# Kernel tuning notes

Hardware: AMD Instinct MI355X
Metric: run time of the kernel (lower is better)

Reference implementation:

```python
import jax, jax.numpy as jnp
import numpy as np

DT = 0.1
THRESH = 10.0

def setup_inputs() -> dict:
    key = jax.random.key(0)
    ks = jax.random.split(key, 6)
    B, S, H, V = 2, 1024, 1024, 50257
    hidden_states = jax.random.normal(ks[0], (B, S, H), dtype=jnp.float32)
    ttu_state = jnp.zeros((B, 3), dtype=jnp.float32)
    W_imp = jax.random.normal(ks[1], (3, H), dtype=jnp.float32) * 0.02
    b_imp = jnp.zeros((3,), dtype=jnp.float32)
    W_lm = jax.random.normal(ks[2], (V, H), dtype=jnp.float32) * 0.02
    W_mod = jax.random.normal(ks[3], (V, 3), dtype=jnp.float32) * 0.02
    # gamma, alpha_c, beta_c, delta, alpha_d, epsilon, alpha_m
    ttu_params = jax.random.uniform(ks[4], (7,), dtype=jnp.float32, minval=0.1, maxval=1.0)
    return {"hidden_states": hidden_states, "ttu_state": ttu_state,
            "W_imp": W_imp, "b_imp": b_imp, "W_lm": W_lm, "W_mod": W_mod,
            "ttu_params": ttu_params}

def _ttu_scan(ttu_state, impulses, ttu_params):
    # impulses: [S, B, 3] (time-major for scan)
    gamma, alpha_c, beta_c, delta, alpha_d, epsilon, alpha_m = ttu_params
    def step(state, imp):
        phi_c, phi_d, phi_m = state[:, 0], state[:, 1], state[:, 2]
        dphi_c = gamma * imp[:, 0] - alpha_c * phi_c - beta_c * phi_c * phi_d
        dphi_d = delta * phi_c ** 2 - alpha_d * phi_d
        dphi_m = epsilon * phi_d - alpha_m * phi_m
        new_c = phi_c + DT * dphi_c
        new_d = phi_d + DT * dphi_d
        new_m = phi_m + DT * dphi_m
        # saturation damping on phi_d
        new_d = jnp.where(jnp.abs(new_d) > THRESH, jnp.float32(0.5), jnp.float32(1.0)) * new_d
        new_state = jnp.stack([new_c, new_d, new_m], axis=1)  # [B, 3]
        return new_state, new_state
    return jax.lax.scan(step, ttu_state, impulses)

def reference(hidden_states, ttu_state, W_imp, b_imp, W_lm, W_mod, ttu_params):
    # impulse projections computed in batch up front: [S, B, 3]
    impulses = jnp.einsum('bsh,dh->sbd', hidden_states, W_imp) + b_imp
    final_state, states = _ttu_scan(ttu_state, impulses, ttu_params)  # states: [S, B, 3]
    # base lm logits + 0.1 * modulation from ttu trajectory
    logits = jnp.einsum('bsh,vh->bsv', hidden_states, W_lm) \
           + 0.1 * jnp.einsum('sbd,vd->bsv', states, W_mod)
    return logits, final_state
```

## Files before the change

kernel.cpp:

```cpp
#include <hip/hip_runtime.h>
#include <hip/hip_bf16.h>

typedef float  f32x4  __attribute__((ext_vector_type(4)));
typedef float  f32x16 __attribute__((ext_vector_type(16)));
typedef short  bf16x8 __attribute__((ext_vector_type(8)));
typedef short  bf16x4 __attribute__((ext_vector_type(4)));

typedef const void __attribute__((address_space(1))) gv_t;
typedef void __attribute__((address_space(3))) sv_t;

namespace {

constexpr int B_ = 2;
constexpr int S_ = 1024;
constexpr int H_ = 1024;
constexpr int V_ = 50257;
constexpr int M_ = B_ * S_;
constexpr int VP2_ = 50432;
constexpr float DT_ = 0.1f;
constexpr float THRESH_ = 10.0f;

constexpr int BK = 64;
constexpr int NT = H_ / BK;

__device__ __forceinline__ unsigned short f2bf(float f) {
  union { float f; unsigned u; } x;
  x.f = f;
  x.u += 0x7FFFu + ((x.u >> 16) & 1u);
  return (unsigned short)(x.u >> 16);
}

__global__ void cvt_hidden_impulse_kernel(const float* __restrict__ hidden,
                                          const float* __restrict__ W_imp,
                                          const float* __restrict__ b_imp,
                                          unsigned short* __restrict__ hid_bf,
                                          float* __restrict__ imp) {
  const int m = blockIdx.x;
  const int t = threadIdx.x;
  const float4 hv = reinterpret_cast<const float4*>(hidden + (size_t)m * H_)[t];
  const float4 wv = reinterpret_cast<const float4*>(W_imp)[t];
  bf16x4 o;
  o[0] = (short)f2bf(hv.x); o[1] = (short)f2bf(hv.y);
  o[2] = (short)f2bf(hv.z); o[3] = (short)f2bf(hv.w);
  *(bf16x4*)(hid_bf + (size_t)m * H_ + t * 4) = o;
  float p = hv.x * wv.x + hv.y * wv.y + hv.z * wv.z + hv.w * wv.w;
  #pragma unroll
  for (int off = 32; off; off >>= 1) p += __shfl_down(p, off);
  __shared__ float partial[4];
  if ((t & 63) == 0) partial[t >> 6] = p;
  __syncthreads();
  if (t == 0) {
    const float v = partial[0] + partial[1] + partial[2] + partial[3] + b_imp[0];
    const int b = m >> 10;
    const int s = m & (S_ - 1);
    imp[s * B_ + b] = v;
  }
}

__device__ __forceinline__ void scan_body(const float* __restrict__ imp_s,
                                          const float* __restrict__ ttu_state,
                                          const float* __restrict__ ttu_params,
                                          float* __restrict__ states,
                                          float* __restrict__ final_out, int t) {
  if (t < B_) {
    const float gamma   = ttu_params[0];
    const float alpha_c = ttu_params[1];
    const float beta_c  = ttu_params[2];
    const float delta   = ttu_params[3];
    const float alpha_d = ttu_params[4];
    const float epsilon = ttu_params[5];
    const float alpha_m = ttu_params[6];
    float c = ttu_state[t * 3 + 0];
    float d = ttu_state[t * 3 + 1];
    float m = ttu_state[t * 3 + 2];
    for (int s = 0; s < S_; ++s) {
      const float ii = imp_s[s * B_ + t];
      const float dc = gamma * ii - alpha_c * c - beta_c * c * d;
      const float dd = delta * c * c - alpha_d * d;
      const float dm = epsilon * d - alpha_m * m;
      c = c + DT_ * dc;
      float nd = d + DT_ * dd;
      m = m + DT_ * dm;
      nd = (fabsf(nd) > THRESH_ ? 0.5f : 1.0f) * nd;
      d = nd;
      float* st = states + (size_t)(s * B_ + t) * 3;
      st[0] = c; st[1] = d; st[2] = m;
    }
    final_out[t * 3 + 0] = c;
    final_out[t * 3 + 1] = d;
    final_out[t * 3 + 2] = m;
  }
}

__global__ void ttu_scan_kernel(const float* __restrict__ imp,
                                const float* __restrict__ ttu_state,
                                const float* __restrict__ ttu_params,
                                float* __restrict__ states,
                                float* __restrict__ final_out) {
  __shared__ float imp_s[S_ * B_];
  const int t = threadIdx.x;
  for (int i = t; i < S_ * B_; i += 64) imp_s[i] = imp[i];
  __syncthreads();
  scan_body(imp_s, ttu_state, ttu_params, states, final_out, t);
}

__global__ void cvt_wlm_scan_kernel(const float* __restrict__ src,
                                    unsigned short* __restrict__ dst,
                                    long n_src, long n_dst,
                                    const float* __restrict__ imp,
                                    const float* __restrict__ ttu_state,
                                    const float* __restrict__ ttu_params,
                                    float* __restrict__ states,
                                    float* __restrict__ final_out) {
  __shared__ float imp_s[S_ * B_];
  const int t = threadIdx.x;
  if (blockIdx.x == gridDim.x - 1) {
    for (int i = t; i < S_ * B_; i += 256) imp_s[i] = imp[i];
    __syncthreads();
    scan_body(imp_s, ttu_state, ttu_params, states, final_out, t);
    return;
  }
  const long stride = (long)(gridDim.x - 1) * blockDim.x * 8;
  for (long i = ((long)blockIdx.x * blockDim.x + t) * 8; i < n_dst; i += stride) {
    bf16x8 v;
    if (i < n_src) {
      const float4 a = *(const float4*)(src + i);
      const float4 b = *(const float4*)(src + i + 4);
      v[0] = (short)f2bf(a.x); v[1] = (short)f2bf(a.y);
      v[2] = (short)f2bf(a.z); v[3] = (short)f2bf(a.w);
      v[4] = (short)f2bf(b.x); v[5] = (short)f2bf(b.y);
      v[6] = (short)f2bf(b.z); v[7] = (short)f2bf(b.w);
    } else {
      v = (bf16x8){0, 0, 0, 0, 0, 0, 0, 0};
    }
    *(bf16x8*)(dst + i) = v;
  }
}

__global__ __launch_bounds__(512, 2) void ttu_gemm_bf16_256w_kernel(
    const unsigned short* __restrict__ Ab,
    const unsigned short* __restrict__ Bb,
    const float* __restrict__ states,
    const float* __restrict__ Wmod,
    float* __restrict__ out)
{
  __shared__ unsigned short A_s[2][256 * BK];
  __shared__ unsigned short B_s[2][256 * BK];
  __shared__ float st_s[256][3];
  __shared__ float wm_s[256][3];

  const int t = threadIdx.x;
  const int cpx = gridDim.x >> 3;
  const int bid = (blockIdx.x & 7) * cpx + (blockIdx.x >> 3);
  const int mb = bid & 7;
  const int nb = bid >> 3;
  const int m0 = mb * 256;
  const int n0 = nb * 256;

  if (t < 256) {
    const int m = m0 + t;
    const int b = m >> 10;
    const int s = m & (S_ - 1);
    const float* st = states + (size_t)(s * B_ + b) * 3;
    st_s[t][0] = st[0]; st_s[t][1] = st[1]; st_s[t][2] = st[2];
  } else {
    const int tt = t - 256;
    const int n = n0 + tt;
    const bool ok = n < V_;
    wm_s[tt][0] = ok ? Wmod[n * 3 + 0] : 0.f;
    wm_s[tt][1] = ok ? Wmod[n * 3 + 1] : 0.f;
    wm_s[tt][2] = ok ? Wmod[n * 3 + 2] : 0.f;
  }

  const int lane = t & 63;
  const int wid  = t >> 6;
  const int lr   = lane >> 3;
  const int ch   = lane & 7;
  const int wmi  = wid >> 2;
  const int wni  = wid & 3;
  const int l31  = lane & 31;
  const int kh   = lane >> 5;

  const unsigned short* Abase = Ab + (size_t)m0 * H_;
  const unsigned short* Bbase = Bb + (size_t)n0 * H_;

  auto STAGE_ALL = [&](int buf, int kt) {
    const int k0 = kt * BK;
    #pragma unroll
    for (int h = 0; h < 4; ++h) {
      const unsigned short* gb = (h < 2) ? Abase : Bbase;
      unsigned short* ls = (h < 2) ? &A_s[buf][0] : &B_s[buf][0];
      const int half = (h & 1) * 128;
      #pragma unroll
      for (int n = 0; n < 2; ++n) {
        const int rbase = half + wid * 16 + n * 8;
        const int r  = rbase + lr;
        const int sc = ch ^ (r & 7);
        __builtin_amdgcn_global_load_lds(
            (gv_t*)(gb + (size_t)r * H_ + k0 + sc * 8),
            (sv_t*)(ls + rbase * BK), 16, 0, 0);
      }
    }
  };

  f32x16 acc[4][2];
  #pragma unroll
  for (int i = 0; i < 4; ++i)
    #pragma unroll
    for (int j = 0; j < 2; ++j)
      acc[i][j] = (f32x16){0.f,0.f,0.f,0.f,0.f,0.f,0.f,0.f,
                           0.f,0.f,0.f,0.f,0.f,0.f,0.f,0.f};

  STAGE_ALL(0, 0);

  int cur = 0;
  for (int kt = 0; kt < NT; ++kt) {
    const int nxt = cur ^ 1;
    asm volatile("s_barrier" ::: "memory");
    if (kt + 1 < NT) {
      STAGE_ALL(nxt, kt + 1);
      asm volatile("s_waitcnt vmcnt(8)" ::: "memory");
    } else {
      asm volatile("s_waitcnt vmcnt(0)" ::: "memory");
    }
    asm volatile("s_barrier" ::: "memory");

    const unsigned short* As = &A_s[cur][0];
    const unsigned short* Bs = &B_s[cur][0];

    bf16x8 bfr[2][4];
    #pragma unroll
    for (int nf = 0; nf < 2; ++nf) {
      const int r = wni * 64 + nf * 32 + l31;
      #pragma unroll
      for (int ks = 0; ks < 4; ++ks)
        bfr[nf][ks] = *(const bf16x8*)&Bs[r * BK + (((ks * 2 + kh) ^ (r & 7)) << 3)];
    }
    bf16x8 af[2][4];
    {
      const int r = wmi * 128 + l31;
      #pragma unroll
      for (int ks = 0; ks < 4; ++ks)
        af[0][ks] = *(const bf16x8*)&As[r * BK + (((ks * 2 + kh) ^ (r & 7)) << 3)];
    }
    #pragma unroll
    for (int mf = 0; mf < 4; ++mf) {
      if (mf < 3) {
        const int r = wmi * 128 + (mf + 1) * 32 + l31;
        #pragma unroll
        for (int ks = 0; ks < 4; ++ks)
          af[(mf + 1) & 1][ks] = *(const bf16x8*)&As[r * BK + (((ks * 2 + kh) ^ (r & 7)) << 3)];
      }
      __builtin_amdgcn_s_setprio(1);
      #pragma unroll
      for (int ks = 0; ks < 4; ++ks)
        #pragma unroll
        for (int nf = 0; nf < 2; ++nf)
          acc[mf][nf] = __builtin_amdgcn_mfma_f32_32x32x16_bf16(
              af[mf & 1][ks], bfr[nf][ks], acc[mf][nf], 0, 0, 0);
      __builtin_amdgcn_s_setprio(0);
    }
    cur ^= 1;
  }

  #pragma unroll
  for (int mf = 0; mf < 4; ++mf) {
    #pragma unroll
    for (int r = 0; r < 16; ++r) {
      const int mloc = wmi * 128 + mf * 32 + (r & 3) + 8 * (r >> 2) + 4 * kh;
      const float s0 = st_s[mloc][0], s1 = st_s[mloc][1], s2 = st_s[mloc][2];
      float* orow = out + (size_t)(m0 + mloc) * V_ + n0;
      #pragma unroll
      for (int nf = 0; nf < 2; ++nf) {
        const int nloc = wni * 64 + nf * 32 + l31;
        if (n0 + nloc < V_) {
          const float corr = 0.1f * (s0 * wm_s[nloc][0] + s1 * wm_s[nloc][1] + s2 * wm_s[nloc][2]);
          orow[nloc] = acc[mf][nf][r] + corr;
        }
      }
    }
  }
}

__global__ __launch_bounds__(256) void ttu_gemm_kernel(
    const float* __restrict__ Ag, const float* __restrict__ Bg,
    const float* __restrict__ states, const float* __restrict__ Wmod,
    float* __restrict__ out)
{
  __shared__ unsigned short A_s[128][40];
  __shared__ unsigned short B_s[128][40];
  __shared__ float st_s[128][3];
  __shared__ float wm_s[128][3];

  const int t   = threadIdx.x;
  const int bid = blockIdx.x;
  const int mb  = bid & 15;
  const int nb  = bid >> 4;
  const int m0  = mb * 128;
  const int n0  = nb * 128;

  if (t < 128) {
    const int m = m0 + t;
    const int b = m >> 10;
    const int s = m & (S_ - 1);
    const float* st = states + (size_t)(s * B_ + b) * 3;
    st_s[t][0] = st[0]; st_s[t][1] = st[1]; st_s[t][2] = st[2];
  } else {
    const int tt = t - 128;
    const int n  = n0 + tt;
    const bool ok = n < V_;
    wm_s[tt][0] = ok ? Wmod[n * 3 + 0] : 0.f;
    wm_s[tt][1] = ok ? Wmod[n * 3 + 1] : 0.f;
    wm_s[tt][2] = ok ? Wmod[n * 3 + 2] : 0.f;
  }

  const int r   = t >> 1;
  const int seg = t & 1;
  const float* arow = Ag + (size_t)(m0 + r) * H_ + seg * 16;
  const int  vrow = n0 + r;
  const bool bok  = vrow < V_;
  const float* brow = Bg + (size_t)(bok ? vrow : 0) * H_ + seg * 16;

  const int lane = t & 63;
  const int wid  = t >> 6;
  const int wm   = wid >> 1;
  const int wn   = wid & 1;
  const int lm   = lane & 15;
  const int kg   = lane >> 4;

  f32x4 acc[4][4];
  #pragma unroll
  for (int i = 0; i < 4; ++i)
    #pragma unroll
    for (int j = 0; j < 4; ++j)
      acc[i][j] = (f32x4){0.f, 0.f, 0.f, 0.f};

  for (int kt = 0; kt < H_ / 32; ++kt) {
    const int k0 = kt * 32;
    const float4 av0 = *(const float4*)(arow + k0 + 0);
    const float4 av1 = *(const float4*)(arow + k0 + 4);
    const float4 av2 = *(const float4*)(arow + k0 + 8);
    const float4 av3 = *(const float4*)(arow + k0 + 12);
    float4 bv0 = {0,0,0,0}, bv1 = {0,0,0,0}, bv2 = {0,0,0,0}, bv3 = {0,0,0,0};
    if (bok) {
      bv0 = *(const float4*)(brow + k0 + 0);
      bv1 = *(const float4*)(brow + k0 + 4);
      bv2 = *(const float4*)(brow + k0 + 8);
      bv3 = *(const float4*)(brow + k0 + 12);
    }
    __syncthreads();
    #define CVT4(v) (bf16x4){(short)f2bf((v).x), (short)f2bf((v).y), (short)f2bf((v).z), (short)f2bf((v).w)}
    *(bf16x4*)&A_s[r][seg * 16 + 0]  = CVT4(av0);
    *(bf16x4*)&A_s[r][seg * 16 + 4]  = CVT4(av1);
    *(bf16x4*)&A_s[r][seg * 16 + 8]  = CVT4(av2);
    *(bf16x4*)&A_s[r][seg * 16 + 12] = CVT4(av3);
    *(bf16x4*)&B_s[r][seg * 16 + 0]  = CVT4(bv0);
    *(bf16x4*)&B_s[r][seg * 16 + 4]  = CVT4(bv1);
    *(bf16x4*)&B_s[r][seg * 16 + 8]  = CVT4(bv2);
    *(bf16x4*)&B_s[r][seg * 16 + 12] = CVT4(bv3);
    #undef CVT4
    __syncthreads();
    bf16x8 af[4], bf[4];
    #pragma unroll
    for (int i = 0; i < 4; ++i) {
      af[i] = *(const bf16x8*)&A_s[wm * 64 + i * 16 + lm][kg * 8];
      bf[i] = *(const bf16x8*)&B_s[wn * 64 + i * 16 + lm][kg * 8];
    }
    #pragma unroll
    for (int i = 0; i < 4; ++i)
      #pragma unroll
      for (int j = 0; j < 4; ++j)
        acc[i][j] = __builtin_amdgcn_mfma_f32_16x16x32_bf16(af[i], bf[j], acc[i][j], 0, 0, 0);
  }

  #pragma unroll
  for (int i = 0; i < 4; ++i) {
    #pragma unroll
    for (int rr = 0; rr < 4; ++rr) {
      const int mloc = wm * 64 + i * 16 + kg * 4 + rr;
      const float s0 = st_s[mloc][0], s1 = st_s[mloc][1], s2 = st_s[mloc][2];
      float* orow = out + (size_t)(m0 + mloc) * V_ + n0;
      #pragma unroll
      for (int j = 0; j < 4; ++j) {
        const int nloc = wn * 64 + j * 16 + lm;
        if (n0 + nloc < V_) {
          const float corr = 0.1f * (s0 * wm_s[nloc][0] + s1 * wm_s[nloc][1] + s2 * wm_s[nloc][2]);
          orow[nloc] = acc[i][j][rr] + corr;
        }
      }
    }
  }
}

}

extern "C" void kernel_launch(void* const* d_in, const int* in_sizes, int n_in,
                              void* d_out, int out_size, void* d_ws, size_t ws_size,
                              hipStream_t stream) {
  const float* hidden     = (const float*)d_in[0];
  const float* ttu_state  = (const float*)d_in[1];
  const float* W_imp      = (const float*)d_in[2];
  const float* b_imp      = (const float*)d_in[3];
  const float* W_lm       = (const float*)d_in[4];
  const float* W_mod      = (const float*)d_in[5];
  const float* ttu_params = (const float*)d_in[6];
  float* out = (float*)d_out;

  float* imp    = (float*)d_ws;
  float* states = imp + S_ * B_;
  float* final_out = out + (size_t)B_ * S_ * V_;

  const size_t need = 32768 + (size_t)M_ * H_ * 2 + (size_t)VP2_ * H_ * 2;

  if (ws_size >= need) {
    unsigned short* hid_bf = (unsigned short*)((char*)d_ws + 32768);
    unsigned short* wlm_bf = hid_bf + (size_t)M_ * H_;
    cvt_hidden_impulse_kernel<<<M_, 256, 0, stream>>>(hidden, W_imp, b_imp, hid_bf, imp);
    cvt_wlm_scan_kernel<<<2049, 256, 0, stream>>>(W_lm, wlm_bf,
                                                  (long)V_ * H_, (long)VP2_ * H_,
                                                  imp, ttu_state, ttu_params,
                                                  states, final_out);
    const int grid = (VP2_ / 256) * (M_ / 256);
    ttu_gemm_bf16_256w_kernel<<<grid, 512, 0, stream>>>(hid_bf, wlm_bf, states, W_mod, out);
  } else {
    cvt_hidden_impulse_kernel<<<M_, 256, 0, stream>>>(hidden, W_imp, b_imp,
                                                      (unsigned short*)d_ws, imp);
    ttu_scan_kernel<<<1, 64, 0, stream>>>(imp, ttu_state, ttu_params, states, final_out);
    const int grid = ((V_ + 127) / 128) * (M_ / 128);
    ttu_gemm_kernel<<<grid, 256, 0, stream>>>(hidden, W_lm, states, W_mod, out);
  }
}
```

Before: 493.4 us.

## Fuse W_lm bf16 conversion into GEMM via register-staged B loads

Removes the separate pass that converted W_lm to a padded bf16 buffer. The GEMM now loads fp32 W_lm rows into registers, converts them to bf16 and writes them to swizzled LDS, with a two-stage prefetch. The MFMA tiling also moves from 32x32x16 to 16x16x32 instructions. The scan goes back to a standalone single-block kernel, which serializes it before the GEMM. In exchange, each M-block re-reads fp32 W_lm (8 times total) at twice the bytes, raises register pressure, and the B path no longer uses direct global-to-LDS loads.

```diff
diff --git a/kernel.cpp b/kernel.cpp
--- a/kernel.cpp
+++ b/kernel.cpp
@@ -2,7 +2,6 @@
 #include <hip/hip_bf16.h>
 
 typedef float  f32x4  __attribute__((ext_vector_type(4)));
-typedef float  f32x16 __attribute__((ext_vector_type(16)));
 typedef short  bf16x8 __attribute__((ext_vector_type(8)));
 typedef short  bf16x4 __attribute__((ext_vector_type(4)));
 
@@ -16,7 +15,6 @@
 constexpr int H_ = 1024;
 constexpr int V_ = 50257;
 constexpr int M_ = B_ * S_;
-constexpr int VP2_ = 50432;
 constexpr float DT_ = 0.1f;
 constexpr float THRESH_ = 10.0f;
 
@@ -57,11 +55,15 @@
   }
 }
 
-__device__ __forceinline__ void scan_body(const float* __restrict__ imp_s,
-                                          const float* __restrict__ ttu_state,
-                                          const float* __restrict__ ttu_params,
-                                          float* __restrict__ states,
-                                          float* __restrict__ final_out, int t) {
+__global__ void ttu_scan_kernel(const float* __restrict__ imp,
+                                const float* __restrict__ ttu_state,
+                                const float* __restrict__ ttu_params,
+                                float* __restrict__ states,
+                                float* __restrict__ final_out) {
+  __shared__ float imp_s[S_ * B_];
+  const int t = threadIdx.x;
+  for (int i = t; i < S_ * B_; i += 64) imp_s[i] = imp[i];
+  __syncthreads();
   if (t < B_) {
     const float gamma   = ttu_params[0];
     const float alpha_c = ttu_params[1];
@@ -92,54 +94,9 @@
   }
 }
 
-__global__ void ttu_scan_kernel(const float* __restrict__ imp,
-                                const float* __restrict__ ttu_state,
-                                const float* __restrict__ ttu_params,
-                                float* __restrict__ states,
-                                float* __restrict__ final_out) {
-  __shared__ float imp_s[S_ * B_];
-  const int t = threadIdx.x;
-  for (int i = t; i < S_ * B_; i += 64) imp_s[i] = imp[i];
-  __syncthreads();
-  scan_body(imp_s, ttu_state, ttu_params, states, final_out, t);
-}
-
-__global__ void cvt_wlm_scan_kernel(const float* __restrict__ src,
-                                    unsigned short* __restrict__ dst,
-                                    long n_src, long n_dst,
-                                    const float* __restrict__ imp,
-                                    const float* __restrict__ ttu_state,
-                                    const float* __restrict__ ttu_params,
-                                    float* __restrict__ states,
-                                    float* __restrict__ final_out) {
-  __shared__ float imp_s[S_ * B_];
-  const int t = threadIdx.x;
-  if (blockIdx.x == gridDim.x - 1) {
-    for (int i = t; i < S_ * B_; i += 256) imp_s[i] = imp[i];
-    __syncthreads();
-    scan_body(imp_s, ttu_state, ttu_params, states, final_out, t);
-    return;
-  }
-  const long stride = (long)(gridDim.x - 1) * blockDim.x * 8;
-  for (long i = ((long)blockIdx.x * blockDim.x + t) * 8; i < n_dst; i += stride) {
-    bf16x8 v;
-    if (i < n_src) {
-      const float4 a = *(const float4*)(src + i);
-      const float4 b = *(const float4*)(src + i + 4);
-      v[0] = (short)f2bf(a.x); v[1] = (short)f2bf(a.y);
-      v[2] = (short)f2bf(a.z); v[3] = (short)f2bf(a.w);
-      v[4] = (short)f2bf(b.x); v[5] = (short)f2bf(b.y);
-      v[6] = (short)f2bf(b.z); v[7] = (short)f2bf(b.w);
-    } else {
-      v = (bf16x8){0, 0, 0, 0, 0, 0, 0, 0};
-    }
-    *(bf16x8*)(dst + i) = v;
-  }
-}
-
-__global__ __launch_bounds__(512, 2) void ttu_gemm_bf16_256w_kernel(
+__global__ __launch_bounds__(512, 2) void ttu_gemm_bf16_regB_kernel(
     const unsigned short* __restrict__ Ab,
-    const unsigned short* __restrict__ Bb,
+    const float* __restrict__ Wlm,
     const float* __restrict__ states,
     const float* __restrict__ Wmod,
     float* __restrict__ out)
@@ -178,104 +135,153 @@
   const int ch   = lane & 7;
   const int wmi  = wid >> 2;
   const int wni  = wid & 3;
-  const int l31  = lane & 31;
-  const int kh   = lane >> 5;
+  const int lm   = lane & 15;
+  const int kg   = lane >> 4;
+
+  const int brl  = t >> 3;
+  const int bseg = t & 7;
 
   const unsigned short* Abase = Ab + (size_t)m0 * H_;
-  const unsigned short* Bbase = Bb + (size_t)n0 * H_;
-
-  auto STAGE_ALL = [&](int buf, int kt) {
+
+  auto STAGE_A = [&](int buf, int kt) {
     const int k0 = kt * BK;
     #pragma unroll
-    for (int h = 0; h < 4; ++h) {
-      const unsigned short* gb = (h < 2) ? Abase : Bbase;
-      unsigned short* ls = (h < 2) ? &A_s[buf][0] : &B_s[buf][0];
-      const int half = (h & 1) * 128;
+    for (int h = 0; h < 2; ++h) {
+      const int half = h * 128;
       #pragma unroll
       for (int n = 0; n < 2; ++n) {
         const int rbase = half + wid * 16 + n * 8;
         const int r  = rbase + lr;
         const int sc = ch ^ (r & 7);
         __builtin_amdgcn_global_load_lds(
-            (gv_t*)(gb + (size_t)r * H_ + k0 + sc * 8),
-            (sv_t*)(ls + rbase * BK), 16, 0, 0);
+            (gv_t*)(Abase + (size_t)r * H_ + k0 + sc * 8),
+            (sv_t*)(&A_s[buf][0] + rbase * BK), 16, 0, 0);
       }
     }
   };
 
-  f32x16 acc[4][2];
+  f32x4 Rb[8];
+  auto LOAD_B = [&](int kt) {
+    const int k0 = kt * BK;
+    #pragma unroll
+    for (int rr = 0; rr < 4; ++rr) {
+      const int g    = n0 + rr * 64 + brl;
+      const int srow = (g < V_) ? g : (V_ - 1);
+      const float* p = Wlm + (size_t)srow * H_ + k0 + bseg * 8;
+      Rb[rr * 2 + 0] = *(const f32x4*)(p);
+      Rb[rr * 2 + 1] = *(const f32x4*)(p + 4);
+    }
+  };
+  auto WRITE_B = [&](int buf) {
+    #pragma unroll
+    for (int rr = 0; rr < 4; ++rr) {
+      const int row = rr * 64 + brl;
+      const bool ok = (n0 + row) < V_;
+      const f32x4 a = Rb[rr * 2 + 0];
+      const f32x4 b = Rb[rr * 2 + 1];
+      bf16x8 o;
+      o[0] = (short)f2bf(a[0]); o[1] = (short)f2bf(a[1]);
+      o[2] = (short)f2bf(a[2]); o[3] = (short)f2bf(a[3]);
+      o[4] = (short)f2bf(b[0]); o[5] = (short)f2bf(b[1]);
+      o[6] = (short)f2bf(b[2]); o[7] = (short)f2bf(b[3]);
+      if (!ok) o = (bf16x8){0, 0, 0, 0, 0, 0, 0, 0};
+      *(bf16x8*)&B_s[buf][row * BK + ((bseg ^ (row & 7)) << 3)] = o;
+    }
+  };
+
+  f32x4 acc[8][4];
   #pragma unroll
-  for (int i = 0; i < 4; ++i)
-    #pragma unroll
-    for (int j = 0; j < 2; ++j)
-      acc[i][j] = (f32x16){0.f,0.f,0.f,0.f,0.f,0.f,0.f,0.f,
-                           0.f,0.f,0.f,0.f,0.f,0.f,0.f,0.f};
-
-  STAGE_ALL(0, 0);
+  for (int i = 0; i < 8; ++i)
+    #pragma unroll
+    for (int j = 0; j < 4; ++j)
+      acc[i][j] = (f32x4){0.f, 0.f, 0.f, 0.f};
+
+  LOAD_B(0);
+  asm volatile("s_waitcnt vmcnt(0)" ::: "memory");
+  WRITE_B(0);
+  LOAD_B(1);
+  STAGE_A(0, 0);
+  asm volatile("s_waitcnt lgkmcnt(0)" ::: "memory");
 
   int cur = 0;
   for (int kt = 0; kt < NT; ++kt) {
     const int nxt = cur ^ 1;
     asm volatile("s_barrier" ::: "memory");
     if (kt + 1 < NT) {
-      STAGE_ALL(nxt, kt + 1);
-      asm volatile("s_waitcnt vmcnt(8)" ::: "memory");
+      asm volatile("s_waitcnt vmcnt(4)" ::: "memory");
+      WRITE_B(nxt);
+      if (kt + 2 < NT) {
+        LOAD_B(kt + 2);
+        STAGE_A(nxt, kt + 1);
+        asm volatile("s_waitcnt vmcnt(12)" ::: "memory");
+      } else {
+        STAGE_A(nxt, kt + 1);
+        asm volatile("s_waitcnt vmcnt(4)" ::: "memory");
+      }
     } else {
       asm volatile("s_waitcnt vmcnt(0)" ::: "memory");
     }
+    asm volatile("s_waitcnt lgkmcnt(0)" ::: "memory");
     asm volatile("s_barrier" ::: "memory");
 
     const unsigned short* As = &A_s[cur][0];
     const unsigned short* Bs = &B_s[cur][0];
 
-    bf16x8 bfr[2][4];
-    #pragma unroll
-    for (int nf = 0; nf < 2; ++nf) {
-      const int r = wni * 64 + nf * 32 + l31;
-      #pragma unroll
-      for (int ks = 0; ks < 4; ++ks)
-        bfr[nf][ks] = *(const bf16x8*)&Bs[r * BK + (((ks * 2 + kh) ^ (r & 7)) << 3)];
-    }
-    bf16x8 af[2][4];
-    {
-      const int r = wmi * 128 + l31;
-      #pragma unroll
-      for (int ks = 0; ks < 4; ++ks)
-        af[0][ks] = *(const bf16x8*)&As[r * BK + (((ks * 2 + kh) ^ (r & 7)) << 3)];
-    }
-    #pragma unroll
-    for (int mf = 0; mf < 4; ++mf) {
-      if (mf < 3) {
-        const int r = wmi * 128 + (mf + 1) * 32 + l31;
+    bf16x8 bfr[4][2];
+    #pragma unroll
+    for (int j = 0; j < 4; ++j)
+      #pragma unroll
+      for (int ks = 0; ks < 2; ++ks) {
+        const int r = wni * 64 + j * 16 + lm;
+        bfr[j][ks] = *(const bf16x8*)&Bs[r * BK + (((ks * 4 + kg) ^ (r & 7)) << 3)];
+      }
+    bf16x8 af[2][2][2];
+    #pragma unroll
+    for (int i2 = 0; i2 < 2; ++i2)
+      #pragma unroll
+      for (int ks = 0; ks < 2; ++ks) {
+        const int r = wmi * 128 + i2 * 16 + lm;
+        af[0][i2][ks] = *(const bf16x8*)&As[r * BK + (((ks * 4 + kg) ^ (r & 7)) << 3)];
+      }
+    #pragma unroll
+    for (int q = 0; q < 4; ++q) {
+      if (q < 3) {
         #pragma unroll
-        for (int ks = 0; ks < 4; ++ks)
-          af[(mf + 1) & 1][ks] = *(const bf16x8*)&As[r * BK + (((ks * 2 + kh) ^ (r & 7)) << 3)];
+        for (int i2 = 0; i2 < 2; ++i2)
+          #pragma unroll
+          for (int ks = 0; ks < 2; ++ks) {
+            const int r = wmi * 128 + ((q + 1) * 2 + i2) * 16 + lm;
+            af[(q + 1) & 1][i2][ks] =
+                *(const bf16x8*)&As[r * BK + (((ks * 4 + kg) ^ (r & 7)) << 3)];
+          }
       }
       __builtin_amdgcn_s_setprio(1);
       #pragma unroll
-      for (int ks = 0; ks < 4; ++ks)
+      for (int ks = 0; ks < 2; ++ks)
         #pragma unroll
-        for (int nf = 0; nf < 2; ++nf)
-          acc[mf][nf] = __builtin_amdgcn_mfma_f32_32x32x16_bf16(
-              af[mf & 1][ks], bfr[nf][ks], acc[mf][nf], 0, 0, 0);
+        for (int i2 = 0; i2 < 2; ++i2)
+          #pragma unroll
+          for (int j = 0; j < 4; ++j)
+            acc[q * 2 + i2][j] = __builtin_amdgcn_mfma_f32_16x16x32_bf16(
+                af[q & 1][i2][ks], bfr[j][ks], acc[q * 2 + i2][j], 0, 0, 0);
       __builtin_amdgcn_s_setprio(0);
     }
     cur ^= 1;
   }
 
   #pragma unroll
-  for (int mf = 0; mf < 4; ++mf) {
-    #pragma unroll
-    for (int r = 0; r < 16; ++r) {
-      const int mloc = wmi * 128 + mf * 32 + (r & 3) + 8 * (r >> 2) + 4 * kh;
+  for (int i = 0; i < 8; ++i) {
+    #pragma unroll
+    for (int rr = 0; rr < 4; ++rr) {
+      const int mloc = wmi * 128 + i * 16 + kg * 4 + rr;
       const float s0 = st_s[mloc][0], s1 = st_s[mloc][1], s2 = st_s[mloc][2];
       float* orow = out + (size_t)(m0 + mloc) * V_ + n0;
       #pragma unroll
-      for (int nf = 0; nf < 2; ++nf) {
-        const int nloc = wni * 64 + nf * 32 + l31;
+      for (int j = 0; j < 4; ++j) {
+        const int nloc = wni * 64 + j * 16 + lm;
         if (n0 + nloc < V_) {
           const float corr = 0.1f * (s0 * wm_s[nloc][0] + s1 * wm_s[nloc][1] + s2 * wm_s[nloc][2]);
-          orow[nloc] = acc[mf][nf][r] + corr;
+          orow[nloc] = acc[i][j][rr] + corr;
         }
       }
     }
@@ -410,18 +416,14 @@
   float* states = imp + S_ * B_;
   float* final_out = out + (size_t)B_ * S_ * V_;
 
-  const size_t need = 32768 + (size_t)M_ * H_ * 2 + (size_t)VP2_ * H_ * 2;
+  const size_t need = 32768 + (size_t)M_ * H_ * 2;
 
   if (ws_size >= need) {
     unsigned short* hid_bf = (unsigned short*)((char*)d_ws + 32768);
-    unsigned short* wlm_bf = hid_bf + (size_t)M_ * H_;
     cvt_hidden_impulse_kernel<<<M_, 256, 0, stream>>>(hidden, W_imp, b_imp, hid_bf, imp);
-    cvt_wlm_scan_kernel<<<2049, 256, 0, stream>>>(W_lm, wlm_bf,
-                                                  (long)V_ * H_, (long)VP2_ * H_,
-                                                  imp, ttu_state, ttu_params,
-                                                  states, final_out);
-    const int grid = (VP2_ / 256) * (M_ / 256);
-    ttu_gemm_bf16_256w_kernel<<<grid, 512, 0, stream>>>(hid_bf, wlm_bf, states, W_mod, out);
+    ttu_scan_kernel<<<1, 64, 0, stream>>>(imp, ttu_state, ttu_params, states, final_out);
+    const int grid = 197 * 8;
+    ttu_gemm_bf16_regB_kernel<<<grid, 512, 0, stream>>>(hid_bf, W_lm, states, W_mod, out);
   } else {
     cvt_hidden_impulse_kernel<<<M_, 256, 0, stream>>>(hidden, W_imp, b_imp,
                                                       (unsigned short*)d_ws, imp);
```

Result: slower. 558.3 us (+13.1%).
